# Optimization experiments

Hardware: AMD Instinct MI355X
Metric: run time of the kernel (lower is better)

Reference implementation:

```python
import jax, jax.numpy as jnp
import numpy as np

N, E, G = 40000, 640000, 256
H, L, FC = 128, 5, 3
Z = 2 * H + 1  # cat([x_i, x_j, edge_attr]) feature dim
OUT = 1


def setup_inputs() -> dict:
    key = jax.random.key(0)
    ks = jax.random.split(key, 12)
    atoms = jax.random.randint(ks[0], (N,), 0, 119)
    pos = jax.random.normal(ks[1], (N, 3), dtype=jnp.float32)
    edge_index = jax.random.randint(ks[2], (2, E), 0, N)
    batch = jnp.sort(jax.random.randint(ks[3], (N,), 0, G))
    s = 1.0 / np.sqrt(Z)
    embed = jax.random.normal(ks[4], (119, H), dtype=jnp.float32) * 0.1
    lin_f_w = jax.random.normal(ks[5], (L, H, Z), dtype=jnp.float32) * s
    lin_f_b = jnp.zeros((L, H), dtype=jnp.float32)
    lin_s_w = jax.random.normal(ks[6], (L, H, Z), dtype=jnp.float32) * s
    lin_s_b = jnp.zeros((L, H), dtype=jnp.float32)
    sh = 1.0 / np.sqrt(H)
    fc_w = jax.random.normal(ks[7], (FC, H, H), dtype=jnp.float32) * sh
    fc_b = jnp.zeros((FC, H), dtype=jnp.float32)
    out_w = jax.random.normal(ks[8], (OUT, H), dtype=jnp.float32) * sh
    out_b = jnp.zeros((OUT,), dtype=jnp.float32)
    return dict(atoms=atoms, pos=pos, edge_index=edge_index, batch=batch,
                embed=embed, lin_f_w=lin_f_w, lin_f_b=lin_f_b,
                lin_s_w=lin_s_w, lin_s_b=lin_s_b,
                fc_w=fc_w, fc_b=fc_b, out_w=out_w, out_b=out_b)


def reference(atoms, pos, edge_index, batch, embed, lin_f_w, lin_f_b,
              lin_s_w, lin_s_b, fc_w, fc_b, out_w, out_b):
    src, dst = edge_index[0], edge_index[1]  # PyG: row0 = source j, row1 = target i
    x = embed[atoms]  # [N,H]
    # edge_attr = ||pos_src - pos_dst|| , shape [E,1]
    ea = jnp.linalg.norm(pos[src] - pos[dst], axis=-1, keepdims=True)
    for l in range(L):
        z = jnp.concatenate([x[dst], x[src], ea], axis=-1)  # [E, 2H+1]
        gate = jax.nn.sigmoid(z @ lin_f_w[l].T + lin_f_b[l])
        core = jax.nn.softplus(z @ lin_s_w[l].T + lin_s_b[l])
        m = gate * core  # [E,H]
        agg = jax.ops.segment_sum(m, dst, num_segments=N)  # scatter-add to targets
        x = x + agg  # CGConv residual
    # mean pooling over graphs
    sums = jax.ops.segment_sum(x, batch, num_segments=G)
    cnt = jax.ops.segment_sum(jnp.ones((x.shape[0], 1), x.dtype), batch, num_segments=G)
    g = sums / jnp.maximum(cnt, 1.0)  # [G,H]
    for l in range(FC):
        g = g @ fc_w[l].T + fc_b[l]
    return g @ out_w.T + out_b  # [G,OUT]
```

## Files before the change

kernel.cpp:

```cpp
#include <hip/hip_runtime.h>
#include <cstdint>
#include <cstddef>

#define N_NODES 40000
#define N_EDGES 640000
#define N_GRAPH 256
#define HDIM 128
#define NLAYERS 5
#define ZDIM 257
#define SCAN_BLOCKS 157

typedef unsigned short ushort8_t __attribute__((ext_vector_type(8)));
typedef short short8 __attribute__((ext_vector_type(8)));
typedef float float4v __attribute__((ext_vector_type(4)));

static __device__ __forceinline__ float bf2f(unsigned short h) {
    return __uint_as_float((unsigned)h << 16);
}
static __device__ __forceinline__ unsigned short f2bf(float f) {
    unsigned u = __float_as_uint(f);
    unsigned r = u + 0x7fffu + ((u >> 16) & 1u);
    return (unsigned short)(r >> 16);
}

__global__ void k_embed(const int* __restrict__ atoms, const float* __restrict__ embed,
                        float* __restrict__ x, unsigned short* __restrict__ xb) {
    int i = blockIdx.x * blockDim.x + threadIdx.x;
    if (i >= N_NODES * 32) return;
    int n = i >> 5, c = i & 31;
    int a = atoms[n];
    float4 v = ((const float4*)embed)[(size_t)a * 32 + c];
    ((float4*)x)[(size_t)n * 32 + c] = v;
    ushort4 w;
    w.x = f2bf(v.x); w.y = f2bf(v.y); w.z = f2bf(v.z); w.w = f2bf(v.w);
    ((ushort4*)xb)[(size_t)n * 32 + c] = w;
}

__global__ void k_hist(const int* __restrict__ ei, int* __restrict__ deg) {
    int e = blockIdx.x * 256 + threadIdx.x;
    if (e >= N_EDGES) return;
    atomicAdd(&deg[ei[N_EDGES + e]], 1);
}

__global__ void k_scan1(const int* __restrict__ deg, int* __restrict__ rowptr,
                        int* __restrict__ bsum) {
    __shared__ int buf[256];
    int tid = threadIdx.x;
    int i = blockIdx.x * 256 + tid;
    int v = (i < N_NODES) ? deg[i] : 0;
    buf[tid] = v;
    __syncthreads();
    for (int off = 1; off < 256; off <<= 1) {
        int t = (tid >= off) ? buf[tid - off] : 0;
        __syncthreads();
        buf[tid] += t;
        __syncthreads();
    }
    if (i < N_NODES) rowptr[i] = buf[tid] - v;
    if (tid == 255) bsum[blockIdx.x] = buf[255];
}

__global__ void k_scan2(int* __restrict__ bsum, int* __restrict__ boff,
                        int* __restrict__ rowptr) {
    __shared__ int buf[256];
    int tid = threadIdx.x;
    int v = (tid < SCAN_BLOCKS) ? bsum[tid] : 0;
    buf[tid] = v;
    __syncthreads();
    for (int off = 1; off < 256; off <<= 1) {
        int t = (tid >= off) ? buf[tid - off] : 0;
        __syncthreads();
        buf[tid] += t;
        __syncthreads();
    }
    if (tid < SCAN_BLOCKS) boff[tid] = buf[tid] - v;
    if (tid == 255) rowptr[N_NODES] = buf[255];
}

__global__ void k_scan3(const int* __restrict__ boff, int* __restrict__ rowptr,
                        int* __restrict__ cursor) {
    int i = blockIdx.x * 256 + threadIdx.x;
    if (i >= N_NODES) return;
    int e = rowptr[i] + boff[blockIdx.x];
    rowptr[i] = e;
    cursor[i] = e;
}

__global__ void k_scatter(const int* __restrict__ ei, const float* __restrict__ pos,
                          int* __restrict__ cursor, int2* __restrict__ csr) {
    int e = blockIdx.x * 256 + threadIdx.x;
    if (e >= N_EDGES) return;
    int s = ei[e], d = ei[N_EDGES + e];
    float dx = pos[3 * s] - pos[3 * d];
    float dy = pos[3 * s + 1] - pos[3 * d + 1];
    float dz = pos[3 * s + 2] - pos[3 * d + 2];
    float ea = sqrtf(dx * dx + dy * dy + dz * dz);
    int p = atomicAdd(&cursor[d], 1);
    csr[p] = make_int2(s, __float_as_int(ea));
}

__global__ void k_gbound(const int* __restrict__ batch, int* __restrict__ gstart) {
    int g = blockIdx.x * 256 + threadIdx.x;
    if (g > N_GRAPH) return;
    if (g == N_GRAPH) { gstart[g] = N_NODES; return; }
    int lo = 0, hi = N_NODES;
    while (lo < hi) {
        int mid = (lo + hi) >> 1;
        if (batch[mid] < g) lo = mid + 1; else hi = mid;
    }
    gstart[g] = lo;
}

__global__ void k_pack(const float* __restrict__ lin_f_w, const float* __restrict__ lin_s_w,
                       unsigned short* __restrict__ Wp, float* __restrict__ wfe,
                       float* __restrict__ wse) {
    int l = blockIdx.y;
    const float* wf = lin_f_w + (size_t)l * HDIM * ZDIM;
    const float* ws = lin_s_w + (size_t)l * HDIM * ZDIM;
    unsigned short* Wpl = Wp + (size_t)l * 512 * 128;
    int i = blockIdx.x * 256 + threadIdx.x;
    if (i < 512 * 128) {
        int n = i >> 7, k = i & 127;
        int blk = n >> 8;
        int cc = n & 255;
        int t = cc & 3;
        int ch = 2 * (cc >> 2) + (t & 1);
        const float* W = (t < 2) ? wf : ws;
        int col = blk ? k : (128 + k);
        Wpl[i] = f2bf(W[ch * ZDIM + col]);
    } else if (i < 512 * 128 + 256) {
        int j = i - 512 * 128;
        if (j < 128) wfe[l * 128 + j] = wf[j * ZDIM + 256];
        else wse[l * 128 + (j - 128)] = ws[(j - 128) * ZDIM + 256];
    }
}

__launch_bounds__(512, 4)
__global__ void k_gemm(const unsigned short* __restrict__ xb,
                       const unsigned short* __restrict__ Wp,
                       const float* __restrict__ bf, const float* __restrict__ bs,
                       unsigned short* __restrict__ P) {
    __shared__ unsigned short smem[32 * 512];
    unsigned short* A = smem;
    const int row0 = blockIdx.x * 64;
    const int tid = threadIdx.x;

    {
        int r = tid >> 3, sub = tid & 7;
        const ushort8_t* src = (const ushort8_t*)(xb + (size_t)(row0 + r) * 128 + sub * 16);
        ushort8_t v0 = src[0], v1 = src[1];
        int h = r & 7;
        *(ushort8_t*)(A + r * 128 + (((sub * 2) ^ h) * 8)) = v0;
        *(ushort8_t*)(A + r * 128 + (((sub * 2 + 1) ^ h) * 8)) = v1;
    }
    __syncthreads();

    const int wid = tid >> 6, lane = tid & 63;
    const int l16 = lane & 15, lg = lane >> 4;

    float4v acc[4][4];
#pragma unroll
    for (int i = 0; i < 4; ++i)
#pragma unroll
        for (int j = 0; j < 4; ++j) acc[i][j] = (float4v){0.f, 0.f, 0.f, 0.f};

#pragma unroll
    for (int ks = 0; ks < 4; ++ks) {
        short8 bfr[4];
#pragma unroll
        for (int cf = 0; cf < 4; ++cf) {
            int n = wid * 64 + cf * 16 + l16;
            bfr[cf] = *(const short8*)(Wp + (size_t)n * 128 + ks * 32 + lg * 8);
        }
#pragma unroll
        for (int rf = 0; rf < 4; ++rf) {
            int row = rf * 16 + l16;
            int kg = ks * 4 + lg;
            short8 af = *(const short8*)(A + row * 128 + ((kg ^ (row & 7)) * 8));
#pragma unroll
            for (int cf = 0; cf < 4; ++cf)
                acc[rf][cf] = __builtin_amdgcn_mfma_f32_16x16x32_bf16(
                    af, bfr[cf], acc[rf][cf], 0, 0, 0);
        }
    }

    float bias[4];
#pragma unroll
    for (int cf = 0; cf < 4; ++cf) {
        int n = wid * 64 + cf * 16 + l16;
        if (n < 256) bias[cf] = 0.f;
        else {
            int cc = n - 256;
            int t = cc & 3;
            int ch = 2 * (cc >> 2) + (t & 1);
            bias[cf] = (t < 2) ? bf[ch] : bs[ch];
        }
    }

#pragma unroll
    for (int p = 0; p < 2; ++p) {
        __syncthreads();
#pragma unroll
        for (int rfl = 0; rfl < 2; ++rfl) {
            int rf = 2 * p + rfl;
#pragma unroll
            for (int cf = 0; cf < 4; ++cf) {
                int col = wid * 64 + cf * 16 + l16;
#pragma unroll
                for (int r = 0; r < 4; ++r) {
                    int rowl = rfl * 16 + lg * 4 + r;
                    smem[rowl * 512 + col] = f2bf(acc[rf][cf][r] + bias[cf]);
                }
            }
        }
        __syncthreads();
#pragma unroll
        for (int i = 0; i < 4; ++i) {
            int u = i * 512 + tid;
            int rw = u >> 6, ch = u & 63;
            *(ushort8_t*)(P + (size_t)(row0 + p * 32 + rw) * 512 + ch * 8) =
                *(const ushort8_t*)(smem + rw * 512 + ch * 8);
        }
    }
}

__launch_bounds__(64)
__global__ void k_edge_csr(const unsigned short* __restrict__ P,
                           const float* __restrict__ wfe, const float* __restrict__ wse,
                           const int* __restrict__ rowptr, const int2* __restrict__ csr,
                           float* __restrict__ x, unsigned short* __restrict__ xb,
                           int node_base) {
    int node = node_base + blockIdx.x;
    int lane = threadIdx.x;
    int beg = rowptr[node], end = rowptr[node + 1];
    ushort4 dv = *(const ushort4*)(P + (size_t)node * 512 + 256 + 4 * lane);
    float fi0 = bf2f(dv.x), fi1 = bf2f(dv.y);
    float si0 = bf2f(dv.z), si1 = bf2f(dv.w);
    float2 wf = ((const float2*)wfe)[lane];
    float2 wsv = ((const float2*)wse)[lane];
    float acc0 = 0.f, acc1 = 0.f;
    const float LOG2E = 1.44269504f, LN2 = 0.69314718f;

    auto edge_math = [&](ushort4 sv, float eav) {
        float g0 = fi0 + bf2f(sv.x) + eav * wf.x;
        float g1 = fi1 + bf2f(sv.y) + eav * wf.y;
        float c0 = si0 + bf2f(sv.z) + eav * wsv.x;
        float c1 = si1 + bf2f(sv.w) + eav * wsv.y;
        float sg0 = __builtin_amdgcn_rcpf(1.f + __builtin_amdgcn_exp2f(-g0 * LOG2E));
        float sg1 = __builtin_amdgcn_rcpf(1.f + __builtin_amdgcn_exp2f(-g1 * LOG2E));
        float a0 = fabsf(c0), a1 = fabsf(c1);
        float l0 = __builtin_amdgcn_logf(1.f + __builtin_amdgcn_exp2f(-a0 * LOG2E)) * LN2;
        float l1 = __builtin_amdgcn_logf(1.f + __builtin_amdgcn_exp2f(-a1 * LOG2E)) * LN2;
        float sp0 = fmaxf(c0, 0.f) + l0;
        float sp1 = fmaxf(c1, 0.f) + l1;
        acc0 += sg0 * sp0;
        acc1 += sg1 * sp1;
    };

    int e = beg;
    for (; e + 4 <= end; e += 4) {
        int2 c0 = csr[e];
        int2 c1 = csr[e + 1];
        int2 c2 = csr[e + 2];
        int2 c3 = csr[e + 3];
        int s0 = __builtin_amdgcn_readfirstlane(c0.x);
        float ea0 = __uint_as_float(__builtin_amdgcn_readfirstlane((unsigned)c0.y));
        int s1 = __builtin_amdgcn_readfirstlane(c1.x);
        float ea1 = __uint_as_float(__builtin_amdgcn_readfirstlane((unsigned)c1.y));
        int s2 = __builtin_amdgcn_readfirstlane(c2.x);
        float ea2 = __uint_as_float(__builtin_amdgcn_readfirstlane((unsigned)c2.y));
        int s3 = __builtin_amdgcn_readfirstlane(c3.x);
        float ea3 = __uint_as_float(__builtin_amdgcn_readfirstlane((unsigned)c3.y));
        ushort4 sv0 = *(const ushort4*)(P + (size_t)s0 * 512 + 4 * lane);
        ushort4 sv1 = *(const ushort4*)(P + (size_t)s1 * 512 + 4 * lane);
        ushort4 sv2 = *(const ushort4*)(P + (size_t)s2 * 512 + 4 * lane);
        ushort4 sv3 = *(const ushort4*)(P + (size_t)s3 * 512 + 4 * lane);
        edge_math(sv0, ea0);
        edge_math(sv1, ea1);
        edge_math(sv2, ea2);
        edge_math(sv3, ea3);
    }
    for (; e < end; ++e) {
        int2 c0 = csr[e];
        int s0 = __builtin_amdgcn_readfirstlane(c0.x);
        float ea0 = __uint_as_float(__builtin_amdgcn_readfirstlane((unsigned)c0.y));
        ushort4 sv0 = *(const ushort4*)(P + (size_t)s0 * 512 + 4 * lane);
        edge_math(sv0, ea0);
    }

    float2* xd = (float2*)(x + (size_t)node * 128) + lane;
    float2 xv = *xd;
    xv.x += acc0;
    xv.y += acc1;
    *xd = xv;
    ushort2 xbv;
    xbv.x = f2bf(xv.x);
    xbv.y = f2bf(xv.y);
    ((ushort2*)(xb + (size_t)node * 128))[lane] = xbv;
}

__launch_bounds__(256)
__global__ void k_poolfc(const float* __restrict__ x, const int* __restrict__ gstart,
                         const float* __restrict__ fc_w, const float* __restrict__ fc_b,
                         const float* __restrict__ out_w, const float* __restrict__ out_b,
                         float* __restrict__ out) {
    int g = blockIdx.x;
    int tid = threadIdx.x;
    int h = tid & 127;
    int half = tid >> 7;
    int s = gstart[g], e = gstart[g + 1];
    float sum = 0.f;
    for (int n = s + half; n < e; n += 2) sum += x[(size_t)n * HDIM + h];
    __shared__ float part[256];
    __shared__ float gin[128];
    __shared__ float gout[128];
    part[tid] = sum;
    __syncthreads();
    float cnt = fmaxf((float)(e - s), 1.0f);
    if (tid < 128) gin[h] = (part[h] + part[h + 128]) / cnt;
    __syncthreads();
    for (int l = 0; l < 3; ++l) {
        float acc = 0.f;
        if (tid < 128) {
            const float* W = fc_w + (size_t)l * HDIM * HDIM + (size_t)h * HDIM;
            acc = fc_b[l * HDIM + h];
#pragma unroll 4
            for (int k = 0; k < HDIM; k += 4) {
                float4 w4 = *(const float4*)(W + k);
                acc += gin[k] * w4.x + gin[k + 1] * w4.y + gin[k + 2] * w4.z + gin[k + 3] * w4.w;
            }
        }
        __syncthreads();
        if (tid < 128) gout[h] = acc;
        __syncthreads();
        if (tid < 128) gin[h] = gout[h];
        __syncthreads();
    }
    if (tid < 128) gout[h] = gin[h] * out_w[h];
    __syncthreads();
    if (tid < 64) gout[tid] += gout[tid + 64];
    __syncthreads();
    if (tid == 0) {
        float acc = 0.f;
        for (int i = 0; i < 64; ++i) acc += gout[i];
        out[g] = acc + out_b[0];
    }
}

extern "C" void kernel_launch(void* const* d_in, const int* in_sizes, int n_in,
                              void* d_out, int out_size, void* d_ws, size_t ws_size,
                              hipStream_t stream) {
    const int* atoms = (const int*)d_in[0];
    const float* pos = (const float*)d_in[1];
    const int* ei = (const int*)d_in[2];
    const int* batch = (const int*)d_in[3];
    const float* embed = (const float*)d_in[4];
    const float* lin_f_w = (const float*)d_in[5];
    const float* lin_f_b = (const float*)d_in[6];
    const float* lin_s_w = (const float*)d_in[7];
    const float* lin_s_b = (const float*)d_in[8];
    const float* fc_w = (const float*)d_in[9];
    const float* fc_b = (const float*)d_in[10];
    const float* out_w = (const float*)d_in[11];
    const float* out_b = (const float*)d_in[12];
    float* out = (float*)d_out;

    char* ws = (char*)d_ws;
    size_t off = 0;
    auto alloc = [&](size_t bytes) -> void* {
        void* p = ws + off;
        off += (bytes + 255) & ~(size_t)255;
        return p;
    };
    float* x            = (float*)alloc((size_t)N_NODES * HDIM * 4);
    unsigned short* xb  = (unsigned short*)alloc((size_t)N_NODES * HDIM * 2);
    unsigned short* P   = (unsigned short*)alloc((size_t)N_NODES * 512 * 2);
    unsigned short* Wp  = (unsigned short*)alloc((size_t)NLAYERS * 512 * 128 * 2);
    float* wfe          = (float*)alloc((size_t)NLAYERS * 128 * 4);
    float* wse          = (float*)alloc((size_t)NLAYERS * 128 * 4);
    int* deg            = (int*)alloc((size_t)N_NODES * 4);
    int* rowptr         = (int*)alloc((size_t)(N_NODES + 1) * 4);
    int* cursor         = (int*)alloc((size_t)N_NODES * 4);
    int* gstart         = (int*)alloc((size_t)(N_GRAPH + 1) * 4);
    int* bsum           = (int*)alloc((size_t)SCAN_BLOCKS * 4);
    int* boff           = (int*)alloc((size_t)SCAN_BLOCKS * 4);
    int2* csr           = (int2*)alloc((size_t)N_EDGES * 8);

    hipMemsetAsync(deg, 0, (size_t)N_NODES * 4, stream);

    k_embed<<<(N_NODES * 32 + 255) / 256, 256, 0, stream>>>(atoms, embed, x, xb);
    k_hist<<<(N_EDGES + 255) / 256, 256, 0, stream>>>(ei, deg);
    k_scan1<<<SCAN_BLOCKS, 256, 0, stream>>>(deg, rowptr, bsum);
    k_scan2<<<1, 256, 0, stream>>>(bsum, boff, rowptr);
    k_scan3<<<SCAN_BLOCKS, 256, 0, stream>>>(boff, rowptr, cursor);
    k_scatter<<<(N_EDGES + 255) / 256, 256, 0, stream>>>(ei, pos, cursor, csr);
    k_gbound<<<2, 256, 0, stream>>>(batch, gstart);
    k_pack<<<dim3(257, NLAYERS), 256, 0, stream>>>(lin_f_w, lin_s_w, Wp, wfe, wse);

    for (int l = 0; l < NLAYERS; ++l) {
        k_gemm<<<625, 512, 0, stream>>>(xb, Wp + (size_t)l * 512 * 128,
                                        lin_f_b + (size_t)l * HDIM,
                                        lin_s_b + (size_t)l * HDIM, P);
        k_edge_csr<<<N_NODES / 2, 64, 0, stream>>>(P, wfe + (size_t)l * 128,
                                                   wse + (size_t)l * 128, rowptr, csr,
                                                   x, xb, 0);
        k_edge_csr<<<N_NODES / 2, 64, 0, stream>>>(P, wfe + (size_t)l * 128,
                                                   wse + (size_t)l * 128, rowptr, csr,
                                                   x, xb, N_NODES / 2);
    }

    k_poolfc<<<N_GRAPH, 256, 0, stream>>>(x, gstart, fc_w, fc_b, out_w, out_b, out);
}
```

Baseline: 529.8 us.

## Merge setup kernels, single edge launch per layer, pad GEMM epilogue smem stride

Fuses the embedding and degree-histogram kernels into one launch, and folds the graph-boundary binary search into the single-block scan kernel. Each layer's two half-range edge launches become one full launch. The GEMM epilogue staging buffer gets a padded row stride of 520 to reduce LDS bank conflicts. Together these cut launch count and shared-memory conflicts, but the fused histogram now runs in blocks sized for the node embedding.

```diff
diff --git a/kernel.cpp b/kernel.cpp
--- a/kernel.cpp
+++ b/kernel.cpp
@@ -9,6 +9,7 @@
 #define NLAYERS 5
 #define ZDIM 257
 #define SCAN_BLOCKS 157
+#define EP_STRIDE 520
 
 typedef unsigned short ushort8_t __attribute__((ext_vector_type(8)));
 typedef short short8 __attribute__((ext_vector_type(8)));
@@ -23,23 +24,22 @@
     return (unsigned short)(r >> 16);
 }
 
-__global__ void k_embed(const int* __restrict__ atoms, const float* __restrict__ embed,
-                        float* __restrict__ x, unsigned short* __restrict__ xb) {
+__global__ void k_embed_hist(const int* __restrict__ atoms, const float* __restrict__ embed,
+                             const int* __restrict__ ei, float* __restrict__ x,
+                             unsigned short* __restrict__ xb, int* __restrict__ deg) {
     int i = blockIdx.x * blockDim.x + threadIdx.x;
-    if (i >= N_NODES * 32) return;
-    int n = i >> 5, c = i & 31;
-    int a = atoms[n];
-    float4 v = ((const float4*)embed)[(size_t)a * 32 + c];
-    ((float4*)x)[(size_t)n * 32 + c] = v;
-    ushort4 w;
-    w.x = f2bf(v.x); w.y = f2bf(v.y); w.z = f2bf(v.z); w.w = f2bf(v.w);
-    ((ushort4*)xb)[(size_t)n * 32 + c] = w;
-}
-
-__global__ void k_hist(const int* __restrict__ ei, int* __restrict__ deg) {
-    int e = blockIdx.x * 256 + threadIdx.x;
-    if (e >= N_EDGES) return;
-    atomicAdd(&deg[ei[N_EDGES + e]], 1);
+    if (i < N_NODES * 32) {
+        int n = i >> 5, c = i & 31;
+        int a = atoms[n];
+        float4 v = ((const float4*)embed)[(size_t)a * 32 + c];
+        ((float4*)x)[(size_t)n * 32 + c] = v;
+        ushort4 w;
+        w.x = f2bf(v.x); w.y = f2bf(v.y); w.z = f2bf(v.z); w.w = f2bf(v.w);
+        ((ushort4*)xb)[(size_t)n * 32 + c] = w;
+    }
+    if (i < N_EDGES) {
+        atomicAdd(&deg[ei[N_EDGES + i]], 1);
+    }
 }
 
 __global__ void k_scan1(const int* __restrict__ deg, int* __restrict__ rowptr,
@@ -60,8 +60,9 @@
     if (tid == 255) bsum[blockIdx.x] = buf[255];
 }
 
-__global__ void k_scan2(int* __restrict__ bsum, int* __restrict__ boff,
-                        int* __restrict__ rowptr) {
+__global__ void k_scan2g(int* __restrict__ bsum, int* __restrict__ boff,
+                         int* __restrict__ rowptr, const int* __restrict__ batch,
+                         int* __restrict__ gstart) {
     __shared__ int buf[256];
     int tid = threadIdx.x;
     int v = (tid < SCAN_BLOCKS) ? bsum[tid] : 0;
@@ -75,6 +76,16 @@
     }
     if (tid < SCAN_BLOCKS) boff[tid] = buf[tid] - v;
     if (tid == 255) rowptr[N_NODES] = buf[255];
+    {
+        int g = tid;
+        int lo = 0, hi = N_NODES;
+        while (lo < hi) {
+            int mid = (lo + hi) >> 1;
+            if (batch[mid] < g) lo = mid + 1; else hi = mid;
+        }
+        gstart[g] = lo;
+        if (tid == 0) gstart[N_GRAPH] = N_NODES;
+    }
 }
 
 __global__ void k_scan3(const int* __restrict__ boff, int* __restrict__ rowptr,
@@ -97,18 +108,6 @@
     float ea = sqrtf(dx * dx + dy * dy + dz * dz);
     int p = atomicAdd(&cursor[d], 1);
     csr[p] = make_int2(s, __float_as_int(ea));
-}
-
-__global__ void k_gbound(const int* __restrict__ batch, int* __restrict__ gstart) {
-    int g = blockIdx.x * 256 + threadIdx.x;
-    if (g > N_GRAPH) return;
-    if (g == N_GRAPH) { gstart[g] = N_NODES; return; }
-    int lo = 0, hi = N_NODES;
-    while (lo < hi) {
-        int mid = (lo + hi) >> 1;
-        if (batch[mid] < g) lo = mid + 1; else hi = mid;
-    }
-    gstart[g] = lo;
 }
 
 __global__ void k_pack(const float* __restrict__ lin_f_w, const float* __restrict__ lin_s_w,
@@ -140,7 +139,7 @@
                        const unsigned short* __restrict__ Wp,
                        const float* __restrict__ bf, const float* __restrict__ bs,
                        unsigned short* __restrict__ P) {
-    __shared__ unsigned short smem[32 * 512];
+    __shared__ unsigned short smem[32 * EP_STRIDE];
     unsigned short* A = smem;
     const int row0 = blockIdx.x * 64;
     const int tid = threadIdx.x;
@@ -209,7 +208,7 @@
 #pragma unroll
                 for (int r = 0; r < 4; ++r) {
                     int rowl = rfl * 16 + lg * 4 + r;
-                    smem[rowl * 512 + col] = f2bf(acc[rf][cf][r] + bias[cf]);
+                    smem[rowl * EP_STRIDE + col] = f2bf(acc[rf][cf][r] + bias[cf]);
                 }
             }
         }
@@ -219,7 +218,7 @@
             int u = i * 512 + tid;
             int rw = u >> 6, ch = u & 63;
             *(ushort8_t*)(P + (size_t)(row0 + p * 32 + rw) * 512 + ch * 8) =
-                *(const ushort8_t*)(smem + rw * 512 + ch * 8);
+                *(const ushort8_t*)(smem + rw * EP_STRIDE + ch * 8);
         }
     }
 }
@@ -228,9 +227,8 @@
 __global__ void k_edge_csr(const unsigned short* __restrict__ P,
                            const float* __restrict__ wfe, const float* __restrict__ wse,
                            const int* __restrict__ rowptr, const int2* __restrict__ csr,
-                           float* __restrict__ x, unsigned short* __restrict__ xb,
-                           int node_base) {
-    int node = node_base + blockIdx.x;
+                           float* __restrict__ x, unsigned short* __restrict__ xb) {
+    int node = blockIdx.x;
     int lane = threadIdx.x;
     int beg = rowptr[node], end = rowptr[node + 1];
     ushort4 dv = *(const ushort4*)(P + (size_t)node * 512 + 256 + 4 * lane);
@@ -388,25 +386,20 @@
 
     hipMemsetAsync(deg, 0, (size_t)N_NODES * 4, stream);
 
-    k_embed<<<(N_NODES * 32 + 255) / 256, 256, 0, stream>>>(atoms, embed, x, xb);
-    k_hist<<<(N_EDGES + 255) / 256, 256, 0, stream>>>(ei, deg);
+    k_embed_hist<<<(N_NODES * 32 + 255) / 256, 256, 0, stream>>>(atoms, embed, ei, x, xb, deg);
     k_scan1<<<SCAN_BLOCKS, 256, 0, stream>>>(deg, rowptr, bsum);
-    k_scan2<<<1, 256, 0, stream>>>(bsum, boff, rowptr);
+    k_scan2g<<<1, 256, 0, stream>>>(bsum, boff, rowptr, batch, gstart);
     k_scan3<<<SCAN_BLOCKS, 256, 0, stream>>>(boff, rowptr, cursor);
     k_scatter<<<(N_EDGES + 255) / 256, 256, 0, stream>>>(ei, pos, cursor, csr);
-    k_gbound<<<2, 256, 0, stream>>>(batch, gstart);
     k_pack<<<dim3(257, NLAYERS), 256, 0, stream>>>(lin_f_w, lin_s_w, Wp, wfe, wse);
 
     for (int l = 0; l < NLAYERS; ++l) {
         k_gemm<<<625, 512, 0, stream>>>(xb, Wp + (size_t)l * 512 * 128,
                                         lin_f_b + (size_t)l * HDIM,
                                         lin_s_b + (size_t)l * HDIM, P);
-        k_edge_csr<<<N_NODES / 2, 64, 0, stream>>>(P, wfe + (size_t)l * 128,
-                                                   wse + (size_t)l * 128, rowptr, csr,
-                                                   x, xb, 0);
-        k_edge_csr<<<N_NODES / 2, 64, 0, stream>>>(P, wfe + (size_t)l * 128,
-                                                   wse + (size_t)l * 128, rowptr, csr,
-                                                   x, xb, N_NODES / 2);
+        k_edge_csr<<<N_NODES, 64, 0, stream>>>(P, wfe + (size_t)l * 128,
+                                               wse + (size_t)l * 128, rowptr, csr,
+                                               x, xb);
     }
 
     k_poolfc<<<N_GRAPH, 256, 0, stream>>>(x, gstart, fc_w, fc_b, out_w, out_b, out);
```

Measured after the change: 487.0 us. 1.09x faster.
